# Kernel tuning notes

Measured on AMD Instinct MI355X. Metric: run time of the kernel, lower is better.

## Reference

```python
import jax, jax.numpy as jnp
import numpy as np

B, V, T = 512, 50257, 2048   # batch, vocab, history length
TOP_K = 50                    # from __init__ arg top_k
NEG_INF = jnp.float32(-1e30)  # finite stand-in for -inf (same softmax result, clean grads)


def setup_inputs() -> dict:
    key = jax.random.key(0)
    k1, k2, k3 = jax.random.split(key, 3)
    logits = jax.random.normal(k1, (B, V), jnp.float32) * 4.0
    previous_tokens = jax.random.randint(k2, (B, T), 0, V)
    # uniform noise for the Gumbel-max trick (torch.rand_like); avoid log(0)
    rand_u = jax.random.uniform(k3, (B, V), jnp.float32, minval=1e-10, maxval=1.0)
    return {
        "logits": logits,
        "previous_tokens": previous_tokens,
        "rand_u": rand_u,
        "temperature": jnp.full((1, 1), 0.8, jnp.float32),
        "top_p": jnp.full((1, 1), 0.8, jnp.float32),
        "repetition_penalty": jnp.full((1, 1), 1.35, jnp.float32),
    }


def _logits_to_probs(logits, previous_tokens, temperature, top_p, repetition_penalty):
    b = jnp.arange(logits.shape[0])[:, None]
    # repetition penalty: gather scores at previous tokens, rescale, scatter back
    score = jnp.take_along_axis(logits, previous_tokens, axis=1)            # [B, T]
    score = jnp.where(score < 0, score * repetition_penalty, score / repetition_penalty)
    logits = logits.at[b, previous_tokens].set(score)
    # top-p (nucleus) filtering: sort descending, cumulative softmax mass
    order = jnp.argsort(-logits, axis=-1)                                   # [B, V]
    sorted_logits = jnp.take_along_axis(logits, order, axis=1)
    cum_probs = jnp.cumsum(jax.nn.softmax(sorted_logits, axis=-1), axis=-1)
    remove_sorted = cum_probs > top_p
    remove_sorted = remove_sorted.at[:, 0].set(False)                       # always keep best token
    # unsort the removal mask back to vocab order (order is a permutation)
    remove = jnp.zeros_like(remove_sorted).at[b, order].set(remove_sorted)
    logits = jnp.where(remove, NEG_INF, logits)
    # temperature
    logits = logits / jnp.maximum(temperature, 1e-5)
    # top-k filtering: mask everything below the k-th largest logit
    v = jax.lax.top_k(logits, TOP_K)[0]                                     # [B, TOP_K]
    pivot = v[:, -1:]
    logits = jnp.where(logits < pivot, NEG_INF, logits)
    return jax.nn.softmax(logits, axis=-1)


def reference(logits, previous_tokens, rand_u, temperature, top_p, repetition_penalty):
    probs = _logits_to_probs(logits, previous_tokens, temperature, top_p, repetition_penalty)
    # Gumbel-max multinomial sample: argmax(probs / Exp(1))
    q = -jnp.log(rand_u)
    idx_next = jnp.argmax(probs / q, axis=-1, keepdims=True).astype(jnp.int64)
    return idx_next, probs
```

## Files before the change

### kernel.cpp

```cpp
#include <hip/hip_runtime.h>
#include <cstdint>
#include <cmath>

#define V_SIZE 50257
#define T_SIZE 2048
#define B_SIZE 512
#define NTHR 512
#define NBINS 512
#define CAND_MAX 1024
#define SPEC_THRESH 10.0f
#define SPEC_MIN 80

__device__ __forceinline__ int bin_of(float x) {
    float t = (32.0f - x) * 8.0f;
    int b = (int)t;
    b = b < 0 ? 0 : b;
    b = b > (NBINS - 1) ? (NBINS - 1) : b;
    return b;
}

extern "C" __global__ __launch_bounds__(NTHR, 4)
void decode_kernel(const float* __restrict__ logits,
                   const int*   __restrict__ prev,
                   const float* __restrict__ rand_u,
                   const float* __restrict__ tempp,
                   const float* __restrict__ toppp,
                   const float* __restrict__ repp,
                   float* __restrict__ out)
{
    const int row  = blockIdx.x;
    const int tid  = threadIdx.x;
    const int lane = tid & 63;
    const int wid  = tid >> 6;

    __shared__ unsigned int bitmap[(V_SIZE + 31) / 32];
    __shared__ int   hist[NBINS];
    __shared__ float cval[CAND_MAX];
    __shared__ int   cidx[CAND_MAX];
    __shared__ float rbuf[CAND_MAX];
    __shared__ float redf[NTHR / 64];
    __shared__ int   redi[NTHR / 64];
    __shared__ float sM, sZ, sS;
    __shared__ int   sCnt, sKc, sSend;

    const float rp   = repp[0];
    const float topp = toppp[0];
    const float temp = fmaxf(tempp[0], 1e-5f);

    const size_t rowoff = (size_t)row * V_SIZE;
    const float* lrow = logits + rowoff;
    const float* urow = rand_u + rowoff;
    float*       orow = out + B_SIZE + rowoff;

    for (int i = tid; i < (V_SIZE + 31) / 32; i += NTHR) bitmap[i] = 0u;
    for (int i = tid; i < NBINS; i += NTHR) hist[i] = 0;
    if (tid == 0) sCnt = 0;
    __syncthreads();

    const int4* prow4 = (const int4*)(prev + (size_t)row * T_SIZE);
    for (int i = tid; i < T_SIZE / 4; i += NTHR) {
        int4 t = prow4[i];
        atomicOr(&bitmap[((unsigned)t.x) >> 5], 1u << (t.x & 31));
        atomicOr(&bitmap[((unsigned)t.y) >> 5], 1u << (t.y & 31));
        atomicOr(&bitmap[((unsigned)t.z) >> 5], 1u << (t.z & 31));
        atomicOr(&bitmap[((unsigned)t.w) >> 5], 1u << (t.w & 31));
    }
    __syncthreads();

    const int head  = (4 - (row & 3)) & 3;
    const int nvec  = (V_SIZE - head) >> 2;
    const int tails = head + nvec * 4;
    const float4* lrow4 = (const float4*)(lrow + head);

    float lm = -INFINITY, lz = 0.0f;
    auto process1 = [&](float x, int v) {
        unsigned w = bitmap[v >> 5];
        if ((w >> (v & 31)) & 1u) x = (x < 0.0f) ? x * rp : x / rp;
        atomicAdd(&hist[bin_of(x)], 1);
        if (x > SPEC_THRESH) {
            int p = atomicAdd(&sCnt, 1);
            if (p < CAND_MAX) { cval[p] = x; cidx[p] = v; }
        }
        if (x > lm) { lz = lz * expf(lm - x) + 1.0f; lm = x; }
        else        { lz += expf(x - lm); }
    };
    if (tid < head)           process1(lrow[tid], tid);
    if (tid < V_SIZE - tails) process1(lrow[tails + tid], tails + tid);
    for (int i = tid; i < nvec; i += NTHR) {
        float4 x4 = lrow4[i];
        int v = head + i * 4;
        process1(x4.x, v); process1(x4.y, v + 1);
        process1(x4.z, v + 2); process1(x4.w, v + 3);
    }

    {
        float wm = lm;
        for (int off = 32; off; off >>= 1) wm = fmaxf(wm, __shfl_down(wm, off));
        if (lane == 0) redf[wid] = wm;
    }
    __syncthreads();
    if (tid == 0) {
        float m = redf[0];
        for (int i = 1; i < NTHR / 64; ++i) m = fmaxf(m, redf[i]);
        sM = m;
    }
    __syncthreads();
    const float M = sM;

    {
        float wz = lz * expf(lm - M);
        for (int off = 32; off; off >>= 1) wz += __shfl_down(wz, off);
        if (lane == 0) redf[wid] = wz;
    }
    __syncthreads();
    if (tid == 0) {
        float z = 0.0f;
        for (int i = 0; i < NTHR / 64; ++i) z += redf[i];
        sZ = z;
    }
    __syncthreads();
    const float Z = sZ;

    {
        float4 z4 = make_float4(0.f, 0.f, 0.f, 0.f);
        if (tid < head)           orow[tid] = 0.0f;
        if (tid < V_SIZE - tails) orow[tails + tid] = 0.0f;
        float4* orow4 = (float4*)(orow + head);
        for (int i = tid; i < nvec; i += NTHR) orow4[i] = z4;
    }

    int cnt = sCnt;
    bool spec_ok = (cnt >= SPEC_MIN && cnt <= CAND_MAX);
    int C;
    if (spec_ok) {
        C = cnt;
    } else {
        if (tid == 0) {
            int cum = 0, kc = NBINS - 1;
            for (int b = 0; b < NBINS; ++b) {
                cum += hist[b];
                if (cum >= SPEC_MIN) { kc = b; break; }
            }
            sKc = kc; sCnt = 0;
        }
        __syncthreads();
        const int kc = sKc;
        auto collect = [&](float x, int v) {
            unsigned w = bitmap[v >> 5];
            if ((w >> (v & 31)) & 1u) x = (x < 0.0f) ? x * rp : x / rp;
            if (bin_of(x) <= kc) {
                int p = atomicAdd(&sCnt, 1);
                if (p < CAND_MAX) { cval[p] = x; cidx[p] = v; }
            }
        };
        if (tid < head)           collect(lrow[tid], tid);
        if (tid < V_SIZE - tails) collect(lrow[tails + tid], tails + tid);
        for (int i = tid; i < nvec; i += NTHR) {
            float4 x4 = lrow4[i];
            int v = head + i * 4;
            collect(x4.x, v); collect(x4.y, v + 1);
            collect(x4.z, v + 2); collect(x4.w, v + 3);
        }
        __syncthreads();
        C = min(sCnt, CAND_MAX);
    }

    int n = 1; while (n < C) n <<= 1;
    for (int i = C + tid; i < n; i += NTHR) { cval[i] = -INFINITY; cidx[i] = 0x7FFFFFFF; }
    __syncthreads();
    for (int k = 2; k <= n; k <<= 1) {
        for (int j = k >> 1; j > 0; j >>= 1) {
            for (int i = tid; i < n; i += NTHR) {
                int l = i ^ j;
                if (l > i) {
                    float vi = cval[i], vl = cval[l];
                    int   ii = cidx[i], il = cidx[l];
                    bool lFirst = (vl > vi) || (vl == vi && il < ii);
                    bool asc = ((i & k) == 0);
                    if (lFirst == asc) {
                        cval[i] = vl; cval[l] = vi;
                        cidx[i] = il; cidx[l] = ii;
                    }
                }
            }
            __syncthreads();
        }
    }

    if (tid == 0) {
        float cum = 0.0f;
        int m = 0;
        float vp = cval[min(49, C - 1)];
        for (int i = 0; i < C; ++i) {
            cum += expf(cval[i] - M) / Z;
            if (i > 0 && cum > topp) break;
            m = i;
            if (m >= 49 && cval[i] < vp) break;
        }
        int send;
        if (m >= 49) {
            int e = 49;
            while (e + 1 < C && cval[e + 1] == vp) ++e;
            send = (m < e) ? m : e;
        } else {
            send = m;
        }
        sSend = send;
    }
    __syncthreads();

    const int send = sSend;
    const float v0 = cval[0];
    for (int i = tid; i <= send; i += NTHR)
        rbuf[i] = expf(cval[i] / temp - v0 / temp);
    __syncthreads();
    if (tid == 0) {
        float S = 0.0f;
        for (int i = 0; i <= send; ++i) S += rbuf[i];
        sS = S;
    }
    __syncthreads();
    const float S = sS;

    float bestr = -1.0f;
    int   besti = 0x7FFFFFFF;
    for (int i = tid; i <= send; i += NTHR) {
        float p = rbuf[i] / S;
        int v = cidx[i];
        orow[v] = p;
        float q = -logf(urow[v]);
        float r = p / q;
        if (r > bestr || (r == bestr && v < besti)) { bestr = r; besti = v; }
    }
    for (int off = 32; off; off >>= 1) {
        float r2 = __shfl_down(bestr, off);
        int   i2 = __shfl_down(besti, off);
        if (r2 > bestr || (r2 == bestr && i2 < besti)) { bestr = r2; besti = i2; }
    }
    if (lane == 0) { redf[wid] = bestr; redi[wid] = besti; }
    __syncthreads();
    if (tid == 0) {
        float br = redf[0]; int bi = redi[0];
        for (int i = 1; i < NTHR / 64; ++i) {
            if (redf[i] > br || (redf[i] == br && redi[i] < bi)) { br = redf[i]; bi = redi[i]; }
        }
        out[row] = (float)bi;
    }
}

extern "C" void kernel_launch(void* const* d_in, const int* in_sizes, int n_in,
                              void* d_out, int out_size, void* d_ws, size_t ws_size,
                              hipStream_t stream) {
    const float* logits = (const float*)d_in[0];
    const int*   prev   = (const int*)d_in[1];
    const float* rand_u = (const float*)d_in[2];
    const float* tempp  = (const float*)d_in[3];
    const float* toppp  = (const float*)d_in[4];
    const float* repp   = (const float*)d_in[5];
    float* out = (float*)d_out;
    hipLaunchKernelGGL(decode_kernel, dim3(B_SIZE), dim3(NTHR), 0, stream,
                       logits, prev, rand_u, tempp, toppp, repp, out);
}
```

Measured before the change: 265.1 us.

## Drop histogram, use fixed-offset softmax sum, fuse zeroing, bisection fallback

Removes the per-element shared-memory histogram atomics from the main pass and replaces the online max/sum softmax with a sum of exp(x - 32) rescaled once by the true max. Output zeroing is fused into the main streaming loop, and the block size doubles to 1024 threads. The rare fallback path, taken when the speculative candidate count is out of range, now bisects on a threshold with repeated counting passes instead of using the histogram. This risks overflow or underflow if logits stray far from the offset, and makes the fallback slower.

```diff
diff --git a/kernel.cpp b/kernel.cpp
--- a/kernel.cpp
+++ b/kernel.cpp
@@ -5,21 +5,14 @@
 #define V_SIZE 50257
 #define T_SIZE 2048
 #define B_SIZE 512
-#define NTHR 512
-#define NBINS 512
+#define NTHR 1024
+#define NWAVE (NTHR / 64)
 #define CAND_MAX 1024
 #define SPEC_THRESH 10.0f
 #define SPEC_MIN 80
-
-__device__ __forceinline__ int bin_of(float x) {
-    float t = (32.0f - x) * 8.0f;
-    int b = (int)t;
-    b = b < 0 ? 0 : b;
-    b = b > (NBINS - 1) ? (NBINS - 1) : b;
-    return b;
-}
-
-extern "C" __global__ __launch_bounds__(NTHR, 4)
+#define KOFF 32.0f
+
+extern "C" __global__ __launch_bounds__(NTHR, 8)
 void decode_kernel(const float* __restrict__ logits,
                    const int*   __restrict__ prev,
                    const float* __restrict__ rand_u,
@@ -34,14 +27,13 @@
     const int wid  = tid >> 6;
 
     __shared__ unsigned int bitmap[(V_SIZE + 31) / 32];
-    __shared__ int   hist[NBINS];
     __shared__ float cval[CAND_MAX];
     __shared__ int   cidx[CAND_MAX];
     __shared__ float rbuf[CAND_MAX];
-    __shared__ float redf[NTHR / 64];
-    __shared__ int   redi[NTHR / 64];
+    __shared__ float redf[NWAVE];
+    __shared__ int   redi[NWAVE];
     __shared__ float sM, sZ, sS;
-    __shared__ int   sCnt, sKc, sSend;
+    __shared__ int   sCnt, sSend;
 
     const float rp   = repp[0];
     const float topp = toppp[0];
@@ -53,7 +45,6 @@
     float*       orow = out + B_SIZE + rowoff;
 
     for (int i = tid; i < (V_SIZE + 31) / 32; i += NTHR) bitmap[i] = 0u;
-    for (int i = tid; i < NBINS; i += NTHR) hist[i] = 0;
     if (tid == 0) sCnt = 0;
     __syncthreads();
 
@@ -71,26 +62,30 @@
     const int nvec  = (V_SIZE - head) >> 2;
     const int tails = head + nvec * 4;
     const float4* lrow4 = (const float4*)(lrow + head);
+    float4*       orow4 = (float4*)(orow + head);
 
     float lm = -INFINITY, lz = 0.0f;
     auto process1 = [&](float x, int v) {
         unsigned w = bitmap[v >> 5];
         if ((w >> (v & 31)) & 1u) x = (x < 0.0f) ? x * rp : x / rp;
-        atomicAdd(&hist[bin_of(x)], 1);
         if (x > SPEC_THRESH) {
             int p = atomicAdd(&sCnt, 1);
             if (p < CAND_MAX) { cval[p] = x; cidx[p] = v; }
         }
-        if (x > lm) { lz = lz * expf(lm - x) + 1.0f; lm = x; }
-        else        { lz += expf(x - lm); }
+        lm = fmaxf(lm, x);
+        lz += __expf(x - KOFF);
     };
-    if (tid < head)           process1(lrow[tid], tid);
-    if (tid < V_SIZE - tails) process1(lrow[tails + tid], tails + tid);
-    for (int i = tid; i < nvec; i += NTHR) {
-        float4 x4 = lrow4[i];
-        int v = head + i * 4;
-        process1(x4.x, v); process1(x4.y, v + 1);
-        process1(x4.z, v + 2); process1(x4.w, v + 3);
+    if (tid < head)           { orow[tid] = 0.0f;          process1(lrow[tid], tid); }
+    if (tid < V_SIZE - tails) { orow[tails + tid] = 0.0f;  process1(lrow[tails + tid], tails + tid); }
+    {
+        float4 z4 = make_float4(0.f, 0.f, 0.f, 0.f);
+        for (int i = tid; i < nvec; i += NTHR) {
+            orow4[i] = z4;
+            float4 x4 = lrow4[i];
+            int v = head + i * 4;
+            process1(x4.x, v); process1(x4.y, v + 1);
+            process1(x4.z, v + 2); process1(x4.w, v + 3);
+        }
     }
 
     {
@@ -101,65 +96,67 @@
     __syncthreads();
     if (tid == 0) {
         float m = redf[0];
-        for (int i = 1; i < NTHR / 64; ++i) m = fmaxf(m, redf[i]);
+        for (int i = 1; i < NWAVE; ++i) m = fmaxf(m, redf[i]);
         sM = m;
     }
     __syncthreads();
     const float M = sM;
 
     {
-        float wz = lz * expf(lm - M);
+        float wz = lz;
         for (int off = 32; off; off >>= 1) wz += __shfl_down(wz, off);
         if (lane == 0) redf[wid] = wz;
     }
     __syncthreads();
     if (tid == 0) {
-        float z = 0.0f;
-        for (int i = 0; i < NTHR / 64; ++i) z += redf[i];
-        sZ = z;
+        float s = 0.0f;
+        for (int i = 0; i < NWAVE; ++i) s += redf[i];
+        sZ = s * expf(KOFF - M);
     }
     __syncthreads();
     const float Z = sZ;
 
-    {
-        float4 z4 = make_float4(0.f, 0.f, 0.f, 0.f);
-        if (tid < head)           orow[tid] = 0.0f;
-        if (tid < V_SIZE - tails) orow[tails + tid] = 0.0f;
-        float4* orow4 = (float4*)(orow + head);
-        for (int i = tid; i < nvec; i += NTHR) orow4[i] = z4;
-    }
-
     int cnt = sCnt;
-    bool spec_ok = (cnt >= SPEC_MIN && cnt <= CAND_MAX);
     int C;
-    if (spec_ok) {
+    if (cnt >= SPEC_MIN && cnt <= CAND_MAX) {
         C = cnt;
     } else {
-        if (tid == 0) {
-            int cum = 0, kc = NBINS - 1;
-            for (int b = 0; b < NBINS; ++b) {
-                cum += hist[b];
-                if (cum >= SPEC_MIN) { kc = b; break; }
+        auto count_pass = [&](float thr) -> int {
+            __syncthreads();
+            if (tid == 0) sCnt = 0;
+            __syncthreads();
+            int local = 0;
+            for (int v = tid; v < V_SIZE; v += NTHR) {
+                float x = lrow[v];
+                unsigned w = bitmap[v >> 5];
+                if ((w >> (v & 31)) & 1u) x = (x < 0.0f) ? x * rp : x / rp;
+                if (x > thr) local++;
             }
-            sKc = kc; sCnt = 0;
-        }
+            if (local) atomicAdd(&sCnt, local);
+            __syncthreads();
+            return sCnt;
+        };
+        float a = -200.0f, b = 200.0f, thr = 0.0f;
+        int c = 0;
+        for (int it = 0; it < 40; ++it) {
+            thr = 0.5f * (a + b);
+            c = count_pass(thr);
+            if (c < SPEC_MIN)       b = thr;
+            else if (c > CAND_MAX)  a = thr;
+            else break;
+        }
+        if (c < SPEC_MIN) thr = a;
         __syncthreads();
-        const int kc = sKc;
-        auto collect = [&](float x, int v) {
+        if (tid == 0) sCnt = 0;
+        __syncthreads();
+        for (int v = tid; v < V_SIZE; v += NTHR) {
+            float x = lrow[v];
             unsigned w = bitmap[v >> 5];
             if ((w >> (v & 31)) & 1u) x = (x < 0.0f) ? x * rp : x / rp;
-            if (bin_of(x) <= kc) {
+            if (x > thr) {
                 int p = atomicAdd(&sCnt, 1);
                 if (p < CAND_MAX) { cval[p] = x; cidx[p] = v; }
             }
-        };
-        if (tid < head)           collect(lrow[tid], tid);
-        if (tid < V_SIZE - tails) collect(lrow[tails + tid], tails + tid);
-        for (int i = tid; i < nvec; i += NTHR) {
-            float4 x4 = lrow4[i];
-            int v = head + i * 4;
-            collect(x4.x, v); collect(x4.y, v + 1);
-            collect(x4.z, v + 2); collect(x4.w, v + 3);
         }
         __syncthreads();
         C = min(sCnt, CAND_MAX);
@@ -241,7 +238,7 @@
     __syncthreads();
     if (tid == 0) {
         float br = redf[0]; int bi = redi[0];
-        for (int i = 1; i < NTHR / 64; ++i) {
+        for (int i = 1; i < NWAVE; ++i) {
             if (redf[i] > br || (redf[i] == br && redi[i] < bi)) { br = redf[i]; bi = redi[i]; }
         }
         out[row] = (float)bi;
```

New measurement: 268.1 us. About the same (+1.1%).
